# Kernel optimization log

Hardware: AMD Instinct MI355X
Metric: run time of the kernel (lower is better)

## Reference

```python
import jax, jax.numpy as jnp
import numpy as np

B = 64            # batch
C = 2             # num_channels (BSF syndrome: X and Z)
L = 64            # lattice size
N = 16            # gradient (histogram) size
BIN = 360 // N    # bin_size = 22 degrees
EPS = 1e-5        # BatchNorm2d default eps


def setup_inputs() -> dict:
    key = jax.random.key(0)
    k1, = jax.random.split(key, 1)
    # syndrome in BSF: binary 0/1 values (torch.nonzero picks the set bits)
    x = jax.random.randint(k1, (B, C * L * L * L), 0, 2).astype(jnp.float32)
    gamma = jnp.ones((C,), jnp.float32)   # BatchNorm2d weight
    beta = jnp.zeros((C,), jnp.float32)   # BatchNorm2d bias
    return {"x": x, "gamma": gamma, "beta": beta}


def _bin_tables():
    # Per lattice site (i,j,k): magnitude and flattened (ax, az) bin index.
    c = jnp.arange(L, dtype=jnp.float32)
    i = c[:, None, None]
    j = c[None, :, None]
    k = c[None, None, :]
    mag = jnp.sqrt(i * i + j * j + k * k)          # (L,L,L)
    x_comp = jnp.sqrt(j * j + k * k)
    z_comp = jnp.sqrt(j * j + i * i)
    deg = 180.0 / jnp.pi
    # atan2 results are in [0, pi] here, so int() truncation == floor
    ax = jnp.floor(jnp.arctan2(x_comp, i) * deg / BIN).astype(jnp.int32)
    az = jnp.floor(jnp.arctan2(k, z_comp) * deg / BIN).astype(jnp.int32)
    bins = (ax * N + az).reshape(-1)               # (L^3,) flattened (ax,az)
    return mag.reshape(-1), bins


def reference(x, gamma, beta):
    mag, bins = _bin_tables()
    # torch.nonzero + indexed update == mask-weighted scatter of magnitudes.
    # x is 0/1, so x * mag equals the mags of the nonzero sites (0 elsewhere).
    xw = x.reshape(B, C, L * L * L) * mag                     # (B,C,L^3)
    g = jnp.zeros((B, C, N * N), x.dtype).at[:, :, bins].add(xw)
    g = g.reshape(B, C, N, N)
    # BatchNorm2d, training mode: per-channel batch statistics (biased var)
    mean = g.mean(axis=(0, 2, 3), keepdims=True)
    var = ((g - mean) ** 2).mean(axis=(0, 2, 3), keepdims=True)
    gn = (g - mean) * jax.lax.rsqrt(var + EPS)
    return gn * gamma[None, :, None, None] + beta[None, :, None, None]
```

## Files before the change

kernel.cpp:

```cpp
#include <hip/hip_runtime.h>


#define BINS_PAD 80

__global__ __launch_bounds__(256)
void bin_table_kernel(unsigned char* __restrict__ tab, float* __restrict__ g) {
    int v = blockIdx.x * 256 + threadIdx.x;
    int i = v >> 12, j = (v >> 6) & 63, k = v & 63;
    double xc2 = (double)(j * j + k * k);
    double zc2 = (double)(i * i + j * j);
    double i2  = (double)(i * i);
    double k2  = (double)(k * k);
    const double T1 = 0.4040262258351568  * 0.4040262258351568;
    const double T2 = 0.9656887748070740  * 0.9656887748070740;
    const double T3 = 2.2460367739042161  * 2.2460367739042161;
    const double T4 = 28.636253282915602  * 28.636253282915602;
    int ax = (xc2 > i2 * T1) + (xc2 > i2 * T2) + (xc2 > i2 * T3) + (xc2 > i2 * T4);
    int az = (k2 > zc2 * T1) + (k2 > zc2 * T2) + (k2 > zc2 * T3) + (k2 > zc2 * T4);
    tab[v] = (unsigned char)(ax * 16 + az);
    if (v < 32768) g[v] = 0.0f;
}

__global__ __launch_bounds__(256)
void scatter_kernel(const float4* __restrict__ x4,
                    const unsigned int* __restrict__ tabu,
                    float* __restrict__ g) {
    __shared__ float hist[BINS_PAD];
    int tid = threadIdx.x;
    int p   = blockIdx.x >> 4;
    int w   = tid >> 6;
    int t   = tid & 63;
    int i   = (blockIdx.x & 15) * 4 + w;
    if (tid < BINS_PAD) hist[tid] = 0.0f;
    __syncthreads();

    const float4*       xs = x4   + (size_t)p * 65536 + (size_t)i * 1024;
    const unsigned int* ts = tabu + i * 1024;

    int thi = t >> 4;
    int k0  = (t & 15) * 4;
    float kk0 = (float)(k0 * k0);
    float kk1 = (float)((k0 + 1) * (k0 + 1));
    float kk2 = (float)((k0 + 2) * (k0 + 2));
    float kk3 = (float)((k0 + 3) * (k0 + 3));
    int i2 = i * i;

    float acc = 0.0f;
    int   cur = 69;

    #pragma unroll 4
    for (int m = 0; m < 16; ++m) {
        float4       xv = xs[m * 64 + t];
        unsigned int u  = ts[m * 64 + t];
        int   j   = m * 4 + thi;
        float r2f = (float)(i2 + j * j);
        {   int b = u & 255;
            float val = xv.x * sqrtf(r2f + kk0);
            if (b != cur) { atomicAdd(&hist[cur], acc); cur = b; acc = val; }
            else          { acc += val; } }
        {   int b = (u >> 8) & 255;
            float val = xv.y * sqrtf(r2f + kk1);
            if (b != cur) { atomicAdd(&hist[cur], acc); cur = b; acc = val; }
            else          { acc += val; } }
        {   int b = (u >> 16) & 255;
            float val = xv.z * sqrtf(r2f + kk2);
            if (b != cur) { atomicAdd(&hist[cur], acc); cur = b; acc = val; }
            else          { acc += val; } }
        {   int b = (u >> 24);
            float val = xv.w * sqrtf(r2f + kk3);
            if (b != cur) { atomicAdd(&hist[cur], acc); cur = b; acc = val; }
            else          { acc += val; } }
    }
    atomicAdd(&hist[cur], acc);
    __syncthreads();

    if (tid < BINS_PAD) {
        float hv = hist[tid];
        if (hv != 0.0f) atomicAdd(&g[p * 256 + tid], hv);
    }
}

__global__ __launch_bounds__(1024)
void norm_kernel(const float* __restrict__ g,
                 const float* __restrict__ gamma,
                 const float* __restrict__ beta,
                 float* __restrict__ out) {
    __shared__ double red[16][4];
    __shared__ float  coef[4];
    int t = threadIdx.x;
    float vals[32];
    double s0 = 0.0, s1 = 0.0, q0 = 0.0, q1 = 0.0;
    #pragma unroll
    for (int n = 0; n < 32; ++n) {
        int idx = t + n * 1024;
        float v = g[idx];
        vals[n] = v;
        double vd = (double)v;
        if ((idx >> 8) & 1) { s1 += vd; q1 += vd * vd; }
        else                { s0 += vd; q0 += vd * vd; }
    }
    #pragma unroll
    for (int off = 32; off > 0; off >>= 1) {
        s0 += __shfl_down(s0, off);
        s1 += __shfl_down(s1, off);
        q0 += __shfl_down(q0, off);
        q1 += __shfl_down(q1, off);
    }
    int wave = t >> 6;
    if ((t & 63) == 0) {
        red[wave][0] = s0; red[wave][1] = s1; red[wave][2] = q0; red[wave][3] = q1;
    }
    __syncthreads();
    if (t == 0) {
        double S0 = 0, S1 = 0, Q0 = 0, Q1 = 0;
        for (int wv = 0; wv < 16; ++wv) {
            S0 += red[wv][0]; S1 += red[wv][1]; Q0 += red[wv][2]; Q1 += red[wv][3];
        }
        const double inv_n = 1.0 / 16384.0;
        double m0 = S0 * inv_n, m1 = S1 * inv_n;
        double v0 = Q0 * inv_n - m0 * m0;
        double v1 = Q1 * inv_n - m1 * m1;
        double r0 = 1.0 / sqrt(v0 + 1e-5);
        double r1 = 1.0 / sqrt(v1 + 1e-5);
        float g0 = gamma[0], g1 = gamma[1], b0 = beta[0], b1 = beta[1];
        coef[0] = (float)r0 * g0;
        coef[1] = (float)r1 * g1;
        coef[2] = b0 - (float)(m0 * r0) * g0;
        coef[3] = b1 - (float)(m1 * r1) * g1;
    }
    __syncthreads();
    float sc0 = coef[0], sc1 = coef[1], sh0 = coef[2], sh1 = coef[3];
    #pragma unroll
    for (int n = 0; n < 32; ++n) {
        int idx = t + n * 1024;
        int c = (idx >> 8) & 1;
        out[idx] = vals[n] * (c ? sc1 : sc0) + (c ? sh1 : sh0);
    }
}

extern "C" void kernel_launch(void* const* d_in, const int* in_sizes, int n_in,
                              void* d_out, int out_size, void* d_ws, size_t ws_size,
                              hipStream_t stream) {
    const float* x     = (const float*)d_in[0];
    const float* gamma = (const float*)d_in[1];
    const float* beta  = (const float*)d_in[2];
    float* out = (float*)d_out;

    unsigned char* tab = (unsigned char*)d_ws;
    float*         g   = (float*)((char*)d_ws + 262144);

    bin_table_kernel<<<1024, 256, 0, stream>>>(tab, g);
    scatter_kernel<<<2048, 256, 0, stream>>>((const float4*)x, (const unsigned int*)tab, g);
    norm_kernel<<<1, 1024, 0, stream>>>(g, gamma, beta, out);
}
```

Before: 208.4 us.

## Fuse batch-norm into scatter kernel via last-block counter; use nontemporal loads

Removes the separate single-block normalization launch. The last scatter block to finish, detected with an atomic counter and thread fences, computes the batch statistics and writes the normalized output using vectorized float4 loads and stores. The input stream is also read with nontemporal loads. This saves one kernel launch and its gap, but adds a global atomic per block, and the final normalization now runs on 256 threads instead of 1024.

```diff
diff --git a/kernel.cpp b/kernel.cpp
--- a/kernel.cpp
+++ b/kernel.cpp
@@ -3,8 +3,11 @@
 
 #define BINS_PAD 80
 
+typedef float vf4 __attribute__((ext_vector_type(4)));
+
 __global__ __launch_bounds__(256)
-void bin_table_kernel(unsigned char* __restrict__ tab, float* __restrict__ g) {
+void bin_table_kernel(unsigned char* __restrict__ tab, float* __restrict__ g,
+                      unsigned int* __restrict__ counter) {
     int v = blockIdx.x * 256 + threadIdx.x;
     int i = v >> 12, j = (v >> 6) & 63, k = v & 63;
     double xc2 = (double)(j * j + k * k);
@@ -19,13 +22,22 @@
     int az = (k2 > zc2 * T1) + (k2 > zc2 * T2) + (k2 > zc2 * T3) + (k2 > zc2 * T4);
     tab[v] = (unsigned char)(ax * 16 + az);
     if (v < 32768) g[v] = 0.0f;
+    if (v == 0)    *counter = 0u;
 }
 
 __global__ __launch_bounds__(256)
-void scatter_kernel(const float4* __restrict__ x4,
-                    const unsigned int* __restrict__ tabu,
-                    float* __restrict__ g) {
+void scatter_norm_kernel(const vf4* __restrict__ x4,
+                         const unsigned int* __restrict__ tabu,
+                         float* __restrict__ g,
+                         unsigned int* __restrict__ counter,
+                         const float* __restrict__ gamma,
+                         const float* __restrict__ beta,
+                         float* __restrict__ out) {
     __shared__ float hist[BINS_PAD];
+    __shared__ unsigned int last_flag;
+    __shared__ double red[4][4];
+    __shared__ float coef[4];
+
     int tid = threadIdx.x;
     int p   = blockIdx.x >> 4;
     int w   = tid >> 6;
@@ -34,7 +46,7 @@
     if (tid < BINS_PAD) hist[tid] = 0.0f;
     __syncthreads();
 
-    const float4*       xs = x4   + (size_t)p * 65536 + (size_t)i * 1024;
+    const vf4*          xs = x4   + (size_t)p * 65536 + (size_t)i * 1024;
     const unsigned int* ts = tabu + i * 1024;
 
     int thi = t >> 4;
@@ -50,7 +62,7 @@
 
     #pragma unroll 4
     for (int m = 0; m < 16; ++m) {
-        float4       xv = xs[m * 64 + t];
+        vf4          xv = __builtin_nontemporal_load(&xs[m * 64 + t]);
         unsigned int u  = ts[m * 64 + t];
         int   j   = m * 4 + thi;
         float r2f = (float)(i2 + j * j);
@@ -78,26 +90,28 @@
         float hv = hist[tid];
         if (hv != 0.0f) atomicAdd(&g[p * 256 + tid], hv);
     }
-}
+    __syncthreads();
 
-__global__ __launch_bounds__(1024)
-void norm_kernel(const float* __restrict__ g,
-                 const float* __restrict__ gamma,
-                 const float* __restrict__ beta,
-                 float* __restrict__ out) {
-    __shared__ double red[16][4];
-    __shared__ float  coef[4];
-    int t = threadIdx.x;
-    float vals[32];
+    if (tid == 0) {
+        __threadfence();
+        unsigned int old = atomicAdd(counter, 1u);
+        last_flag = (old == 2047u);
+    }
+    __syncthreads();
+    if (!last_flag) return;
+
+    __threadfence();
+    const vf4* g4 = (const vf4*)g;
     double s0 = 0.0, s1 = 0.0, q0 = 0.0, q1 = 0.0;
     #pragma unroll
     for (int n = 0; n < 32; ++n) {
-        int idx = t + n * 1024;
-        float v = g[idx];
-        vals[n] = v;
-        double vd = (double)v;
-        if ((idx >> 8) & 1) { s1 += vd; q1 += vd * vd; }
-        else                { s0 += vd; q0 += vd * vd; }
+        int idx = tid + n * 256;
+        vf4 v = g4[idx];
+        double a = v.x, b = v.y, c = v.z, d = v.w;
+        double sum = a + b + c + d;
+        double sq  = a * a + b * b + c * c + d * d;
+        if ((idx >> 6) & 1) { s1 += sum; q1 += sq; }
+        else                { s0 += sum; q0 += sq; }
     }
     #pragma unroll
     for (int off = 32; off > 0; off >>= 1) {
@@ -106,14 +120,11 @@
         q0 += __shfl_down(q0, off);
         q1 += __shfl_down(q1, off);
     }
-    int wave = t >> 6;
-    if ((t & 63) == 0) {
-        red[wave][0] = s0; red[wave][1] = s1; red[wave][2] = q0; red[wave][3] = q1;
-    }
+    if (t == 0) { red[w][0] = s0; red[w][1] = s1; red[w][2] = q0; red[w][3] = q1; }
     __syncthreads();
-    if (t == 0) {
+    if (tid == 0) {
         double S0 = 0, S1 = 0, Q0 = 0, Q1 = 0;
-        for (int wv = 0; wv < 16; ++wv) {
+        for (int wv = 0; wv < 4; ++wv) {
             S0 += red[wv][0]; S1 += red[wv][1]; Q0 += red[wv][2]; Q1 += red[wv][3];
         }
         const double inv_n = 1.0 / 16384.0;
@@ -130,11 +141,17 @@
     }
     __syncthreads();
     float sc0 = coef[0], sc1 = coef[1], sh0 = coef[2], sh1 = coef[3];
+    vf4* out4 = (vf4*)out;
     #pragma unroll
     for (int n = 0; n < 32; ++n) {
-        int idx = t + n * 1024;
-        int c = (idx >> 8) & 1;
-        out[idx] = vals[n] * (c ? sc1 : sc0) + (c ? sh1 : sh0);
+        int idx = tid + n * 256;
+        vf4 v = g4[idx];
+        int c = (idx >> 6) & 1;
+        float sc = c ? sc1 : sc0, sh = c ? sh1 : sh0;
+        vf4 o;
+        o.x = v.x * sc + sh; o.y = v.y * sc + sh;
+        o.z = v.z * sc + sh; o.w = v.w * sc + sh;
+        out4[idx] = o;
     }
 }
 
@@ -146,10 +163,11 @@
     const float* beta  = (const float*)d_in[2];
     float* out = (float*)d_out;
 
-    unsigned char* tab = (unsigned char*)d_ws;
-    float*         g   = (float*)((char*)d_ws + 262144);
+    unsigned char* tab     = (unsigned char*)d_ws;
+    float*         g       = (float*)((char*)d_ws + 262144);
+    unsigned int*  counter = (unsigned int*)((char*)d_ws + 393216);
 
-    bin_table_kernel<<<1024, 256, 0, stream>>>(tab, g);
-    scatter_kernel<<<2048, 256, 0, stream>>>((const float4*)x, (const unsigned int*)tab, g);
-    norm_kernel<<<1, 1024, 0, stream>>>(g, gamma, beta, out);
+    bin_table_kernel<<<1024, 256, 0, stream>>>(tab, g, counter);
+    scatter_norm_kernel<<<2048, 256, 0, stream>>>((const vf4*)x, (const unsigned int*)tab,
+                                                  g, counter, gamma, beta, out);
 }
```

Result: slower. 293.1 us (+40.6%).
